# Kernel optimization log

Hardware: AMD Instinct MI355X
Metric: run time of the kernel (lower is better)

Reference implementation:

```python
import jax, jax.numpy as jnp
import numpy as np

N_NODES = 50000
N_EDGES = 800000
NUM_IN, NUM_OUT, NUM_HID, NUM_MSG = 1, 1, 30, 200


def _linear_params(key, fan_in, fan_out):
    k1, k2 = jax.random.split(key)
    s = 1.0 / np.sqrt(fan_in)
    W = jax.random.uniform(k1, (fan_in, fan_out), jnp.float32, -s, s)
    b = jax.random.uniform(k2, (fan_out,), jnp.float32, -s, s)
    return W, b


def _layer_params(key, c_in, c_out, c_msg):
    ks = jax.random.split(key, 4)
    W1, b1 = _linear_params(ks[0], c_in, c_out)          # lin_1
    Wm1, bm1 = _linear_params(ks[1], 2 * c_in + 2, c_msg)  # mlp[0]
    Wm2, bm2 = _linear_params(ks[2], c_msg, c_in)          # mlp[2]
    W2, b2 = _linear_params(ks[3], c_in, c_out)          # lin_2
    return W1, b1, Wm1, bm1, Wm2, bm2, W2, b2


def setup_inputs() -> dict:
    key = jax.random.key(0)
    ks = jax.random.split(key, 6)
    features = jax.random.normal(ks[0], (N_NODES, NUM_IN), jnp.float32)
    edges = jax.random.randint(ks[1], (2, N_EDGES), 0, N_NODES, jnp.int64)
    weights = jax.random.normal(ks[2], (N_EDGES, 2), jnp.float32)
    inp = {"features": features, "edges": edges, "weights": weights}
    names = ["W1", "b1", "Wm1", "bm1", "Wm2", "bm2", "W2", "b2"]
    for suf, kk, (ci, co) in zip(["d", "h", "o"], ks[3:6],
                                 [(NUM_IN, NUM_HID), (NUM_HID, NUM_HID), (NUM_HID, NUM_OUT)]):
        ps = _layer_params(kk, ci, co, NUM_MSG)
        for nm, p in zip(names, ps):
            inp[f"{nm}_{suf}"] = p
    return inp


def _mpd(x, src, dst, ea, W1, b1, Wm1, bm1, Wm2, bm2, W2, b2):
    # PyG default flow source_to_target: x_j = x[src], x_i = x[dst], aggregate to dst
    xi = x[dst]
    xj = x[src]
    tmp = jnp.concatenate([xi, xj, ea], axis=1)            # [E, 2*in+2]
    h = jax.nn.relu(tmp @ Wm1 + bm1)                       # [E, msg]
    m = h @ Wm2 + bm2                                      # [E, in]
    msg = (m * (xi - xj)) @ W2 + b2                        # [E, out]
    agg = jax.ops.segment_sum(msg, dst, num_segments=x.shape[0])
    return agg + x @ W1 + b1


def reference(features, edges, weights,
              W1_d, b1_d, Wm1_d, bm1_d, Wm2_d, bm2_d, W2_d, b2_d,
              W1_h, b1_h, Wm1_h, bm1_h, Wm2_h, bm2_h, W2_h, b2_h,
              W1_o, b1_o, Wm1_o, bm1_o, Wm2_o, bm2_o, W2_o, b2_o):
    src, dst = edges[0], edges[1]
    x = jax.nn.relu(_mpd(features, src, dst, weights,
                         W1_d, b1_d, Wm1_d, bm1_d, Wm2_d, bm2_d, W2_d, b2_d))
    for _ in range(3):
        x = jax.nn.relu(_mpd(x, src, dst, weights,
                             W1_h, b1_h, Wm1_h, bm1_h, Wm2_h, bm2_h, W2_h, b2_h))
    return _mpd(x, src, dst, weights,
                W1_o, b1_o, Wm1_o, bm1_o, Wm2_o, bm2_o, W2_o, b2_o)
```

## Files before the change

### kernel.cpp

```cpp
#include <hip/hip_runtime.h>

#define N_NODES 50000
#define N_EDGES 800000
#define C_MSG 200

typedef __bf16 bf16;
typedef __attribute__((ext_vector_type(8))) __bf16 bf16x8;
typedef __attribute__((ext_vector_type(4))) float f32x4;

static __device__ __forceinline__ unsigned int pk_bf16(float a, float b) {
    union { bf16 h[2]; unsigned int u; } cv;
    cv.h[0] = (bf16)a; cv.h[1] = (bf16)b;
    return cv.u;
}

static __device__ __forceinline__ f32x4 MF(bf16x8 a, bf16x8 b, f32x4 c) {
    return __builtin_amdgcn_mfma_f32_16x16x32_bf16(a, b, c, 0, 0, 0);
}

static __device__ void dev_pack_wm1(int tid, const float* W, const float* bm1,
                                    bf16* out) {
    int i = tid & 7, lane = (tid >> 3) & 63, rest = tid >> 9;
    int kt = rest % 2, t = rest / 2;
    int k = kt * 32 + ((lane >> 4) * 8) + i;
    int c = lane & 15;
    int n = (t < 12) ? ((t >> 1) * 32 + 2 * c + (t & 1)) : (192 + c);
    float v = 0.f;
    if (n < C_MSG) {
        if (k < 30)       v = W[k * C_MSG + n];
        else if (k == 30) v = bm1[n];
        else if (k >= 32) v = W[(k - 2) * C_MSG + n];
    }
    out[tid] = (bf16)v;
}

static __device__ void dev_pack_wm2(int tid, const float* W, const float* bm2,
                                    bf16* out) {
    int i = tid & 7, lane = (tid >> 3) & 63, rest = tid >> 9;
    int kt = rest % 7, nt = rest / 7;
    int k = kt * 32 + ((lane >> 4) * 8) + i;
    int n = 2 * (lane & 15) + nt;
    float v = 0.f;
    if (n < 30) {
        if (k < C_MSG)       v = W[k * 30 + n];
        else if (k == C_MSG) v = bm2[n];
    }
    out[tid] = (bf16)v;
}

static __device__ void dev_pack_w2h(int tid, const float* W, const float* b2,
                                    bf16* out) {
    int i = tid & 7, lane = (tid >> 3) & 63, nt = tid >> 9;
    int k = ((lane >> 4) * 8) + i;
    int n = 2 * (lane & 15) + nt;
    float v = 0.f;
    if (n < 30) {
        if (k < 30)       v = W[k * 30 + n];
        else if (k == 30) v = b2[n];
    }
    out[tid] = (bf16)v;
}

static __device__ void dev_pack_w2o(int tid, const float* W, const float* b2,
                                    bf16* out) {
    int i = tid & 7, lane = (tid >> 3) & 63;
    int k = ((lane >> 4) * 8) + i;
    int n = lane & 15;
    float v = 0.f;
    if (n == 0) {
        if (k < 30)       v = W[k];
        else if (k == 30) v = b2[0];
    }
    out[tid] = (bf16)v;
}

static __device__ void dev_pack_sel(int tid, bf16* out) {
    int i = tid & 7, lane = (tid >> 3) & 63, f = tid >> 9;
    int kt = f >> 1, nt = f & 1;
    int kloc = ((lane >> 4) * 8) + i;
    int n = 2 * (lane & 15) + nt;
    float v = (kloc == n && n < 30) ? ((kt & 1) ? -1.f : 1.f) : 0.f;
    out[tid] = (bf16)v;
}

__global__ __launch_bounds__(256) void setup_a(
    const int* __restrict__ dst, int* __restrict__ counts,
    const float* __restrict__ Wm1_h, const float* __restrict__ bm1_h,
    const float* __restrict__ Wm1_o, const float* __restrict__ bm1_o,
    const float* __restrict__ Wm2_h, const float* __restrict__ bm2_h,
    const float* __restrict__ Wm2_o, const float* __restrict__ bm2_o,
    const float* __restrict__ W2_h,  const float* __restrict__ b2_h,
    const float* __restrict__ W2_o,  const float* __restrict__ b2_o,
    const float* __restrict__ Wm1_d,
    bf16* __restrict__ Wm1B_h, bf16* __restrict__ Wm1B_o,
    bf16* __restrict__ Wm2B_h, bf16* __restrict__ Wm2B_o,
    bf16* __restrict__ W2B_h,  bf16* __restrict__ W2B_o,
    bf16* __restrict__ SelB,   float* __restrict__ Wm1T_d,
    const float* __restrict__ features, const float* __restrict__ W1_d,
    const float* __restrict__ b1_d, float* __restrict__ bufA) {
    int b = blockIdx.x, t = threadIdx.x;
    if (b < 3125) {
        int e = b * 256 + t;
        if (e < N_EDGES) atomicAdd(&counts[dst[e]], 1);
    } else if (b < 3311) {
        int pb = b - 3125;
        if (pb < 52)       dev_pack_wm1(pb * 256 + t, Wm1_h, bm1_h, Wm1B_h);
        else if (pb < 104) dev_pack_wm1((pb - 52) * 256 + t, Wm1_o, bm1_o, Wm1B_o);
        else if (pb < 132) dev_pack_wm2((pb - 104) * 256 + t, Wm2_h, bm2_h, Wm2B_h);
        else if (pb < 160) dev_pack_wm2((pb - 132) * 256 + t, Wm2_o, bm2_o, Wm2B_o);
        else if (pb < 164) dev_pack_w2h((pb - 160) * 256 + t, W2_h, b2_h, W2B_h);
        else if (pb < 166) dev_pack_w2o((pb - 164) * 256 + t, W2_o, b2_o, W2B_o);
        else if (pb < 182) dev_pack_sel((pb - 166) * 256 + t, SelB);
        else {
            int i = (pb - 182) * 256 + t;
            if (i < C_MSG * 4) Wm1T_d[i] = Wm1_d[(i & 3) * C_MSG + (i >> 2)];
        }
    } else {
        int n = (b - 3311) * 256 + t;
        if (n < N_NODES) {
            float xv = features[n];
            for (int o = 0; o < 30; ++o)
                bufA[n * 30 + o] = fmaf(xv, W1_d[o], b1_d[o]);
        }
    }
}

__global__ __launch_bounds__(256) void scan_kernel(const int* __restrict__ counts,
                                                   int* __restrict__ offsets,
                                                   int* __restrict__ cursor) {
    __shared__ int ws[4];
    const int b = blockIdx.x, t = threadIdx.x;
    const int lane = t & 63, wv = t >> 6;
    int acc = 0;
    for (int i = t; i < b * 256; i += 256) acc += counts[i];
#pragma unroll
    for (int d = 32; d > 0; d >>= 1) acc += __shfl_xor(acc, d);
    if (lane == 0) ws[wv] = acc;
    __syncthreads();
    int base = ws[0] + ws[1] + ws[2] + ws[3];
    __syncthreads();
    int i = b * 256 + t;
    int v = (i < N_NODES) ? counts[i] : 0;
    int inc = v;
#pragma unroll
    for (int d = 1; d < 64; d <<= 1) {
        int u = __shfl_up(inc, d);
        if (lane >= d) inc += u;
    }
    if (lane == 63) ws[wv] = inc;
    __syncthreads();
    int waveoff = 0;
    for (int k = 0; k < wv; ++k) waveoff += ws[k];
    int excl = base + waveoff + inc - v;
    if (i < N_NODES) { offsets[i] = excl; cursor[i] = excl; }
    if (i == N_NODES - 1) offsets[N_NODES] = excl + v;
}

__global__ __launch_bounds__(256) void scatter_kernel(
    const int* __restrict__ src, const int* __restrict__ dst,
    const float* __restrict__ ew, int* __restrict__ cursor,
    int4* __restrict__ edata, float2* __restrict__ ewp) {
    int e = blockIdx.x * 256 + threadIdx.x;
    if (e < N_EDGES) {
        int d = dst[e];
        float e0 = ew[2 * e], e1 = ew[2 * e + 1];
        int p = atomicAdd(&cursor[d], 1);
        edata[p] = make_int4(src[e], d, (int)pk_bf16(e0, e1), e);
        ewp[p] = make_float2(e0, e1);
    }
}

__global__ __launch_bounds__(256) void edge_d_kernel(
    const float* __restrict__ x, const int4* __restrict__ edata,
    const float2* __restrict__ ewp,
    const float* __restrict__ Wm1T, const float* __restrict__ bm1,
    const float* __restrict__ Wm2, const float* __restrict__ bm2,
    const float* __restrict__ W2, const float* __restrict__ b2, bf16* __restrict__ msg)
{
    int t = blockIdx.x * 256 + threadIdx.x;
    int4 ed = edata[t];
    float xi = x[ed.y], xj = x[ed.x];
    float2 e01 = ewp[t];
    float e0 = e01.x, e1 = e01.y;
    float m = bm2[0];
    for (int j = 0; j < C_MSG; ++j) {
        const float* __restrict__ wr = Wm1T + j * 4;
        float h = bm1[j];
        h = fmaf(xi, wr[0], h);
        h = fmaf(xj, wr[1], h);
        h = fmaf(e0, wr[2], h);
        h = fmaf(e1, wr[3], h);
        h = fmaxf(h, 0.f);
        m = fmaf(h, Wm2[j], m);
    }
    float md = m * (xi - xj);
    for (int o = 0; o < 15; ++o) {
        float f0 = fmaf(md, W2[2 * o], b2[2 * o]);
        float f1 = fmaf(md, W2[2 * o + 1], b2[2 * o + 1]);
        *(unsigned int*)(msg + (size_t)t * 32 + 2 * o) = pk_bf16(f0, f1);
    }
}


#define LOAD_FRAGS(P, ED) do {                                                \
    const bf16* rd_ = xc + (size_t)(ED).y * 64 + quad * 8;                    \
    const bf16* rs_ = xc + (size_t)(ED).x * 64 + quad * 8;                    \
    P##A0 = *(const bf16x8*)(rd_);                                            \
    P##a2 = *(const bf16x8*)(rd_ + 32);                                       \
    P##A1 = *(const bf16x8*)(rs_);                                            \
    P##a3 = *(const bf16x8*)(rs_ + 32);                                       \
} while (0)

#define COMPUTE_TILE(P, EDZ, EBASE) do {                                      \
    if (quad == 3) {                                                          \
        union { unsigned int u; bf16 b[2]; } cv_;                             \
        cv_.u = (unsigned int)(EDZ);                                          \
        P##A1[6] = cv_.b[0];                                                  \
        P##A1[7] = cv_.b[1];                                                  \
    }                                                                         \
               \
    f32x4 m0_ = {0.f,0.f,0.f,0.f}, m1_ = {0.f,0.f,0.f,0.f};                   \
    _Pragma("unroll")                                                         \
    for (int p_ = 0; p_ < 6; ++p_) {                                          \
        char* cb_ = (p_ & 1) ? cB : cA;                                       \
        const bf16* Wf_ = Wm1L + (4 * p_) * 512 + lane * 8;                   \
        bf16x8 be0_ = *(const bf16x8*)(Wf_);                                  \
        bf16x8 be1_ = *(const bf16x8*)(Wf_ + 512);                            \
        bf16x8 bo0_ = *(const bf16x8*)(Wf_ + 1024);                           \
        bf16x8 bo1_ = *(const bf16x8*)(Wf_ + 1536);                           \
        f32x4 ae_ = {0.f,0.f,0.f,0.f}, ao_ = {0.f,0.f,0.f,0.f};               \
        ae_ = MF(P##A0, be0_, ae_);                                           \
        ae_ = MF(P##A1, be1_, ae_);                                           \
        ao_ = MF(P##A0, bo0_, ao_);                                           \
        ao_ = MF(P##A1, bo1_, ao_);                                           \
        _Pragma("unroll")                                                     \
        for (int rg_ = 0; rg_ < 4; ++rg_) {                                   \
            int row_ = row0 + rg_, wb_ = 4 * col;                             \
            unsigned int u_ = pk_bf16(fmaxf(ae_[rg_],0.f), fmaxf(ao_[rg_],0.f)); \
            *(unsigned int*)(cb_ + row_ * 64 + ((wb_ & 48) ^ ((row_ & 3) << 4)) \
                             + (wb_ & 15)) = u_;                              \
        }                                                                     \
        bf16x8 a_ = *(const bf16x8*)(cb_ + col * 64 +                         \
                                     ((quad << 4) ^ ((col & 3) << 4)));       \
        m0_ = MF(a_, *(const bf16x8*)(Wm2L + p_ * 512 + lane * 8), m0_);      \
        m1_ = MF(a_, *(const bf16x8*)(Wm2L + (7 + p_) * 512 + lane * 8), m1_);\
    }                                                                         \
    {     \
        const bf16* Wf_ = Wm1L + 24 * 512 + lane * 8;                         \
        bf16x8 b0_ = *(const bf16x8*)(Wf_);                                   \
        bf16x8 b1_ = *(const bf16x8*)(Wf_ + 512);                             \
        f32x4 acc_ = {0.f,0.f,0.f,0.f};                                       \
        acc_ = MF(P##A0, b0_, acc_);                                          \
        acc_ = MF(P##A1, b1_, acc_);                                          \
        if (col < 8) {                                                        \
            _Pragma("unroll")                                                 \
            for (int rg_ = 0; rg_ < 4; ++rg_) {                               \
                int row_ = row0 + rg_;                                        \
                *(bf16*)(cP + row_ * 64 + ((row_ & 3) << 4) + 2 * col) =      \
                    (bf16)fmaxf(acc_[rg_], 0.f);                              \
            }                                                                 \
        }                                                                     \
        bf16x8 a_ = *(const bf16x8*)(cP + col * 64 +                          \
                                     ((quad << 4) ^ ((col & 3) << 4)));       \
        m0_ = MF(a_, *(const bf16x8*)(Wm2L + 6 * 512 + lane * 8), m0_);       \
        m1_ = MF(a_, *(const bf16x8*)(Wm2L + 13 * 512 + lane * 8), m1_);      \
    }                                                                         \
          \
    f32x4 dc0_ = {0.f,0.f,0.f,0.f}, dc1_ = {0.f,0.f,0.f,0.f};                 \
    dc0_ = MF(P##A0, *(const bf16x8*)(SelB + (size_t)0*512 + lane*8), dc0_);  \
    dc1_ = MF(P##A0, *(const bf16x8*)(SelB + (size_t)1*512 + lane*8), dc1_);  \
    dc0_ = MF(P##A1, *(const bf16x8*)(SelB + (size_t)2*512 + lane*8), dc0_);  \
    dc1_ = MF(P##A1, *(const bf16x8*)(SelB + (size_t)3*512 + lane*8), dc1_);  \
    dc0_ = MF(P##a2, *(const bf16x8*)(SelB + (size_t)4*512 + lane*8), dc0_);  \
    dc1_ = MF(P##a2, *(const bf16x8*)(SelB + (size_t)5*512 + lane*8), dc1_);  \
    dc0_ = MF(P##a3, *(const bf16x8*)(SelB + (size_t)6*512 + lane*8), dc0_);  \
    dc1_ = MF(P##a3, *(const bf16x8*)(SelB + (size_t)7*512 + lane*8), dc1_);  \
                                   \
    _Pragma("unroll")                                                         \
    for (int rg_ = 0; rg_ < 4; ++rg_) {                                       \
        int row_ = row0 + rg_, wb_ = 4 * col;                                 \
        unsigned int u_ = (col == 15) ? pk_bf16(1.f, 0.f)                     \
                        : pk_bf16(m0_[rg_]*dc0_[rg_], m1_[rg_]*dc1_[rg_]);    \
        *(unsigned int*)(cA + row_ * 64 + ((wb_ & 48) ^ ((row_ & 3) << 4))    \
                         + (wb_ & 15)) = u_;                                  \
    }                                                                         \
    bf16x8 am_ = *(const bf16x8*)(cA + col * 64 +                             \
                                  ((quad << 4) ^ ((col & 3) << 4)));          \
                                      \
    if (COUT == 30) {                                                         \
        f32x4 c0_ = {0.f,0.f,0.f,0.f}, c1_ = {0.f,0.f,0.f,0.f};               \
        c0_ = MF(am_, *(const bf16x8*)(W2B + lane*8), c0_);                   \
        c1_ = MF(am_, *(const bf16x8*)(W2B + 512 + lane*8), c1_);             \
        _Pragma("unroll")                                                     \
        for (int rg_ = 0; rg_ < 4; ++rg_)                                     \
            *(unsigned int*)(msg + (size_t)((EBASE) + row0 + rg_)*32 + 2*col) = \
                pk_bf16(c0_[rg_], c1_[rg_]);                                  \
    } else {                                                                  \
                  \
        f32x4 c0_ = {0.f,0.f,0.f,0.f};                                        \
        c0_ = MF(am_, *(const bf16x8*)(W2B + lane*8), c0_);                   \
        if (col == 0) {                                                       \
            union { bf16 h[4]; unsigned long long u; } pk4_;                  \
            _Pragma("unroll")                                                 \
            for (int rg_ = 0; rg_ < 4; ++rg_) pk4_.h[rg_] = (bf16)c0_[rg_];   \
            *(unsigned long long*)(msg + ((EBASE) + row0)) = pk4_.u;          \
        }                                                                     \
    }                                                                         \
} while (0)

template<int COUT>
__global__ __launch_bounds__(256, 3) void edge_mfma(
    const bf16* __restrict__ xc, const int4* __restrict__ edata,
    const bf16* __restrict__ Wm1B, const bf16* __restrict__ SelB,
    const bf16* __restrict__ Wm2B, const bf16* __restrict__ W2B,
    bf16* __restrict__ msg)
{
    __shared__ __align__(16) bf16 smem[26624];
    bf16* Wm1L = smem;
    bf16* Wm2L = smem + 13312;

    const int tid = threadIdx.x, w = tid >> 6, lane = tid & 63;
    const int col = lane & 15, quad = lane >> 4, row0 = quad * 4;
    const int myrow = w * 16;
    const int blk = blockIdx.x * 256;

    const int eoff = myrow + col;
    int4 ed0 = edata[blk + 0 * 64 + eoff];
    int4 ed1 = edata[blk + 1 * 64 + eoff];
    int4 ed2 = edata[blk + 2 * 64 + eoff];
    int4 ed3 = edata[blk + 3 * 64 + eoff];

#pragma unroll
    for (int i = 0; i < 10; ++i) {
        int idx = tid + i * 256;
        bf16x8 v = (idx < 1664) ? *((const bf16x8*)Wm1B + idx)
                                : *((const bf16x8*)Wm2B + (idx - 1664));
        *((bf16x8*)smem + idx) = v;
    }
    __syncthreads();

    char* cbase = (char*)(smem + 20480 + w * 1536);
    char* cA = cbase;
    char* cB = cbase + 1024;
    char* cP = cbase + 2048;

    if (lane < 48) {
        int r = lane / 3, s = 1 + (lane - r * 3);
        bf16x8 z = {};
        if (s == 1) z[0] = (bf16)1.f;
        *(bf16x8*)(cP + r * 64 + ((s << 4) ^ ((r & 3) << 4))) = z;
    }

    bf16x8 pA0, pA1, pa2, pa3, qA0, qA1, qa2, qa3;
    LOAD_FRAGS(p, ed0);
    LOAD_FRAGS(q, ed1);

    COMPUTE_TILE(p, ed0.z, blk + 0 * 64 + myrow);
    LOAD_FRAGS(p, ed2);
    COMPUTE_TILE(q, ed1.z, blk + 1 * 64 + myrow);
    LOAD_FRAGS(q, ed3);
    COMPUTE_TILE(p, ed2.z, blk + 2 * 64 + myrow);
    COMPUTE_TILE(q, ed3.z, blk + 3 * 64 + myrow);
}

template<int CNEXT>
__global__ __launch_bounds__(256) void agg_fused(
    const bf16* __restrict__ msg, const int* __restrict__ offsets,
    const float* __restrict__ bufc,
    const float* __restrict__ W1n, const float* __restrict__ b1n,
    float* __restrict__ bufn,
    bf16* __restrict__ xc) {
    int gh = (blockIdx.x * 256 + threadIdx.x) >> 4;
    int lane = threadIdx.x & 15;
    int s0 = offsets[gh], s1 = offsets[gh + 1];
    float r0 = 0.f, r1 = 0.f;
    if (lane < 15) {
        float v0 = 0.f, v1 = 0.f;
        const unsigned int* mp =
            (const unsigned int*)(msg + (size_t)s0 * 32 + lane * 2);
        int cnt = s1 - s0, j = 0;
        for (; j + 4 <= cnt; j += 4) {
            unsigned int u0 = mp[(size_t)(j + 0) * 16];
            unsigned int u1 = mp[(size_t)(j + 1) * 16];
            unsigned int u2 = mp[(size_t)(j + 2) * 16];
            unsigned int u3 = mp[(size_t)(j + 3) * 16];
            union { unsigned int u; bf16 b[2]; } c0, c1, c2, c3;
            c0.u = u0; c1.u = u1; c2.u = u2; c3.u = u3;
            v0 += (float)c0.b[0]; v1 += (float)c0.b[1];
            v0 += (float)c1.b[0]; v1 += (float)c1.b[1];
            v0 += (float)c2.b[0]; v1 += (float)c2.b[1];
            v0 += (float)c3.b[0]; v1 += (float)c3.b[1];
        }
        for (; j < cnt; ++j) {
            union { unsigned int u; bf16 b[2]; } cv;
            cv.u = mp[(size_t)j * 16];
            v0 += (float)cv.b[0]; v1 += (float)cv.b[1];
        }
        float f0 = bufc[(size_t)gh * 30 + 2 * lane] + v0;
        float f1 = bufc[(size_t)gh * 30 + 2 * lane + 1] + v1;
        r0 = fmaxf(f0, 0.f);
        r1 = fmaxf(f1, 0.f);
        bf16 h0 = (bf16)r0, h1 = (bf16)r1;
        union { bf16 h[2]; unsigned int u; } hi;
        hi.h[0] = h0; hi.h[1] = h1;
        *(unsigned int*)(xc + (size_t)gh * 64 + 2 * lane) = hi.u;
        *(unsigned int*)(xc + (size_t)gh * 64 + 32 + 2 * lane) =
            pk_bf16(r0 - (float)h0, r1 - (float)h1);
    } else {
        *(unsigned int*)(xc + (size_t)gh * 64 + 30) = pk_bf16(1.f, 0.f);
        *(unsigned int*)(xc + (size_t)gh * 64 + 62) = 0u;
    }
    if (CNEXT == 30) {
        float acc0 = 0.f, acc1 = 0.f;
        if (lane < 15) { acc0 = b1n[2 * lane]; acc1 = b1n[2 * lane + 1]; }
        for (int k2 = 0; k2 < 15; ++k2) {
            float rk0 = __shfl(r0, k2, 16);
            float rk1 = __shfl(r1, k2, 16);
            if (lane < 15) {
                const float* w0 = W1n + (2 * k2) * 30 + 2 * lane;
                const float* w1 = W1n + (2 * k2 + 1) * 30 + 2 * lane;
                acc0 = fmaf(rk0, w0[0], acc0);
                acc1 = fmaf(rk0, w0[1], acc1);
                acc0 = fmaf(rk1, w1[0], acc0);
                acc1 = fmaf(rk1, w1[1], acc1);
            }
        }
        if (lane < 15) {
            bufn[(size_t)gh * 30 + 2 * lane] = acc0;
            bufn[(size_t)gh * 30 + 2 * lane + 1] = acc1;
        }
    } else {
        float acc = b1n[0];
        for (int k2 = 0; k2 < 15; ++k2) {
            float rk0 = __shfl(r0, k2, 16);
            float rk1 = __shfl(r1, k2, 16);
            acc = fmaf(rk0, W1n[2 * k2], acc);
            acc = fmaf(rk1, W1n[2 * k2 + 1], acc);
        }
        if (lane == 0) bufn[gh] = acc;
    }
}

__global__ __launch_bounds__(256) void agg_last(const bf16* __restrict__ msg1,
                                                const int* __restrict__ offsets,
                                                float* __restrict__ out) {
    int gh = (blockIdx.x * 256 + threadIdx.x) >> 5;
    int lane = threadIdx.x & 31;
    int s0 = offsets[gh], s1 = offsets[gh + 1];
    float v = 0.f;
    for (int j = s0 + lane; j < s1; j += 32) v += (float)msg1[j];
#pragma unroll
    for (int o = 16; o > 0; o >>= 1) v += __shfl_xor(v, o);
    if (lane == 0) out[gh] += v;
}

extern "C" void kernel_launch(void* const* d_in, const int* in_sizes, int n_in,
                              void* d_out, int out_size, void* d_ws, size_t ws_size,
                              hipStream_t stream) {
    const float* features = (const float*)d_in[0];
    const int*   edges    = (const int*)d_in[1];
    const float* ew       = (const float*)d_in[2];

    const float* W1_d  = (const float*)d_in[3];
    const float* b1_d  = (const float*)d_in[4];
    const float* Wm1_d = (const float*)d_in[5];
    const float* bm1_d = (const float*)d_in[6];
    const float* Wm2_d = (const float*)d_in[7];
    const float* bm2_d = (const float*)d_in[8];
    const float* W2_d  = (const float*)d_in[9];
    const float* b2_d  = (const float*)d_in[10];

    const float* W1_h  = (const float*)d_in[11];
    const float* b1_h  = (const float*)d_in[12];
    const float* Wm1_h = (const float*)d_in[13];
    const float* bm1_h = (const float*)d_in[14];
    const float* Wm2_h = (const float*)d_in[15];
    const float* bm2_h = (const float*)d_in[16];
    const float* W2_h  = (const float*)d_in[17];
    const float* b2_h  = (const float*)d_in[18];

    const float* W1_o  = (const float*)d_in[19];
    const float* b1_o  = (const float*)d_in[20];
    const float* Wm1_o = (const float*)d_in[21];
    const float* bm1_o = (const float*)d_in[22];
    const float* Wm2_o = (const float*)d_in[23];
    const float* bm2_o = (const float*)d_in[24];
    const float* W2_o  = (const float*)d_in[25];
    const float* b2_o  = (const float*)d_in[26];

    const int* src = edges;
    const int* dst = edges + N_EDGES;
    float* out = (float*)d_out;

    char* p = (char*)d_ws;
    auto alloc = [&](size_t bytes) { char* r = p; p += (bytes + 63) & ~(size_t)63; return r; };
    float* bufA    = (float*)alloc((size_t)N_NODES * 30 * 4);
    float* bufB    = (float*)alloc((size_t)N_NODES * 30 * 4);
    bf16*  msg     = (bf16*) alloc((size_t)N_EDGES * 32 * 2);
    bf16*  xc      = (bf16*) alloc((size_t)N_NODES * 64 * 2);
    int*   counts  = (int*)  alloc((size_t)N_NODES * 4);
    int*   offsets = (int*)  alloc((size_t)(N_NODES + 1) * 4);
    int*   cursor  = (int*)  alloc((size_t)N_NODES * 4);
    int4*  edata   = (int4*) alloc((size_t)N_EDGES * 16);
    float2* ewp    = (float2*)alloc((size_t)N_EDGES * 8);
    float* Wm1T_d  = (float*)alloc((size_t)C_MSG * 4 * 4);
    bf16*  Wm1B_h  = (bf16*) alloc((size_t)26 * 512 * 2);
    bf16*  Wm1B_o  = (bf16*) alloc((size_t)26 * 512 * 2);
    bf16*  Wm2B_h  = (bf16*) alloc((size_t)14 * 512 * 2);
    bf16*  Wm2B_o  = (bf16*) alloc((size_t)14 * 512 * 2);
    bf16*  W2B_h   = (bf16*) alloc((size_t)2 * 512 * 2);
    bf16*  W2B_o   = (bf16*) alloc((size_t)1 * 512 * 2);
    bf16*  SelB    = (bf16*) alloc((size_t)8 * 512 * 2);

    hipMemsetAsync(counts, 0, (size_t)N_NODES * 4, stream);
    setup_a<<<3507, 256, 0, stream>>>(dst, counts,
        Wm1_h, bm1_h, Wm1_o, bm1_o, Wm2_h, bm2_h, Wm2_o, bm2_o,
        W2_h, b2_h, W2_o, b2_o, Wm1_d,
        Wm1B_h, Wm1B_o, Wm2B_h, Wm2B_o, W2B_h, W2B_o, SelB, Wm1T_d,
        features, W1_d, b1_d, bufA);
    scan_kernel<<<(N_NODES + 255) / 256, 256, 0, stream>>>(counts, offsets, cursor);
    scatter_kernel<<<N_EDGES / 256, 256, 0, stream>>>(src, dst, ew, cursor, edata, ewp);

    dim3 tb(256);
    dim3 eb_mfma(N_EDGES / 256);
    dim3 eb_valu(N_EDGES / 256);
    dim3 ab16(N_NODES * 16 / 256);
    dim3 ab32(N_NODES * 32 / 256);

    edge_d_kernel<<<eb_valu, tb, 0, stream>>>(features, edata, ewp,
        Wm1T_d, bm1_d, Wm2_d, bm2_d, W2_d, b2_d, msg);
    agg_fused<30><<<ab16, tb, 0, stream>>>(msg, offsets, bufA, W1_h, b1_h, bufB, xc);

    edge_mfma<30><<<eb_mfma, tb, 0, stream>>>(xc, edata,
        Wm1B_h, SelB, Wm2B_h, W2B_h, msg);
    agg_fused<30><<<ab16, tb, 0, stream>>>(msg, offsets, bufB, W1_h, b1_h, bufA, xc);

    edge_mfma<30><<<eb_mfma, tb, 0, stream>>>(xc, edata,
        Wm1B_h, SelB, Wm2B_h, W2B_h, msg);
    agg_fused<30><<<ab16, tb, 0, stream>>>(msg, offsets, bufA, W1_h, b1_h, bufB, xc);

    edge_mfma<30><<<eb_mfma, tb, 0, stream>>>(xc, edata,
        Wm1B_h, SelB, Wm2B_h, W2B_h, msg);
    agg_fused<1><<<ab16, tb, 0, stream>>>(msg, offsets, bufB, W1_o, b1_o, out, xc);

    edge_mfma<1><<<eb_mfma, tb, 0, stream>>>(xc, edata,
        Wm1B_o, SelB, Wm2B_o, W2B_o, msg);
    agg_last<<<ab32, tb, 0, stream>>>(msg, offsets, out);
}
```

Baseline: 581.6 us.

## Double edges per MFMA block, stage layer-d weights in LDS, unroll aggregation

The MFMA edge kernel now handles 512 edges per block instead of 256, so the LDS weight preload and setup are amortized over twice as many tiles. The edata and msg buffers are padded and zero-filled so the last block can safely read past the edge count. The first-layer VALU edge kernel stages its MLP weights in shared memory instead of reading them from global memory inside the loop. The aggregation loop gains an 8-way unrolled path for more loads in flight. In exchange, the MFMA grid halves, which lowers parallelism and extends each block's serial chain of tiles.

```diff
diff --git a/kernel.cpp b/kernel.cpp
--- a/kernel.cpp
+++ b/kernel.cpp
@@ -177,21 +177,33 @@
     const float* __restrict__ Wm2, const float* __restrict__ bm2,
     const float* __restrict__ W2, const float* __restrict__ b2, bf16* __restrict__ msg)
 {
+    __shared__ float sw[C_MSG * 6 + 1];
+    for (int i = threadIdx.x; i < C_MSG * 6 + 1; i += 256) {
+        float v;
+        if (i < C_MSG * 4)            v = Wm1T[i];
+        else if (i < C_MSG * 5)       v = bm1[i - C_MSG * 4];
+        else if (i < C_MSG * 6)       v = Wm2[i - C_MSG * 5];
+        else                          v = bm2[0];
+        sw[i] = v;
+    }
+    __syncthreads();
+
     int t = blockIdx.x * 256 + threadIdx.x;
     int4 ed = edata[t];
     float xi = x[ed.y], xj = x[ed.x];
     float2 e01 = ewp[t];
     float e0 = e01.x, e1 = e01.y;
-    float m = bm2[0];
+    float m = sw[C_MSG * 6];
+#pragma unroll 4
     for (int j = 0; j < C_MSG; ++j) {
-        const float* __restrict__ wr = Wm1T + j * 4;
-        float h = bm1[j];
+        const float* wr = sw + j * 4;
+        float h = sw[C_MSG * 4 + j];
         h = fmaf(xi, wr[0], h);
         h = fmaf(xj, wr[1], h);
         h = fmaf(e0, wr[2], h);
         h = fmaf(e1, wr[3], h);
         h = fmaxf(h, 0.f);
-        m = fmaf(h, Wm2[j], m);
+        m = fmaf(h, sw[C_MSG * 5 + j], m);
     }
     float md = m * (xi - xj);
     for (int o = 0; o < 15; ++o) {
@@ -322,13 +334,17 @@
     const int tid = threadIdx.x, w = tid >> 6, lane = tid & 63;
     const int col = lane & 15, quad = lane >> 4, row0 = quad * 4;
     const int myrow = w * 16;
-    const int blk = blockIdx.x * 256;
+    const int blk = blockIdx.x * 512;
 
     const int eoff = myrow + col;
     int4 ed0 = edata[blk + 0 * 64 + eoff];
     int4 ed1 = edata[blk + 1 * 64 + eoff];
     int4 ed2 = edata[blk + 2 * 64 + eoff];
     int4 ed3 = edata[blk + 3 * 64 + eoff];
+    int4 ed4 = edata[blk + 4 * 64 + eoff];
+    int4 ed5 = edata[blk + 5 * 64 + eoff];
+    int4 ed6 = edata[blk + 6 * 64 + eoff];
+    int4 ed7 = edata[blk + 7 * 64 + eoff];
 
 #pragma unroll
     for (int i = 0; i < 10; ++i) {
@@ -360,7 +376,15 @@
     COMPUTE_TILE(q, ed1.z, blk + 1 * 64 + myrow);
     LOAD_FRAGS(q, ed3);
     COMPUTE_TILE(p, ed2.z, blk + 2 * 64 + myrow);
+    LOAD_FRAGS(p, ed4);
     COMPUTE_TILE(q, ed3.z, blk + 3 * 64 + myrow);
+    LOAD_FRAGS(q, ed5);
+    COMPUTE_TILE(p, ed4.z, blk + 4 * 64 + myrow);
+    LOAD_FRAGS(p, ed6);
+    COMPUTE_TILE(q, ed5.z, blk + 5 * 64 + myrow);
+    LOAD_FRAGS(q, ed7);
+    COMPUTE_TILE(p, ed6.z, blk + 6 * 64 + myrow);
+    COMPUTE_TILE(q, ed7.z, blk + 7 * 64 + myrow);
 }
 
 template<int CNEXT>
@@ -379,6 +403,27 @@
         const unsigned int* mp =
             (const unsigned int*)(msg + (size_t)s0 * 32 + lane * 2);
         int cnt = s1 - s0, j = 0;
+        for (; j + 8 <= cnt; j += 8) {
+            unsigned int u0 = mp[(size_t)(j + 0) * 16];
+            unsigned int u1 = mp[(size_t)(j + 1) * 16];
+            unsigned int u2 = mp[(size_t)(j + 2) * 16];
+            unsigned int u3 = mp[(size_t)(j + 3) * 16];
+            unsigned int u4 = mp[(size_t)(j + 4) * 16];
+            unsigned int u5 = mp[(size_t)(j + 5) * 16];
+            unsigned int u6 = mp[(size_t)(j + 6) * 16];
+            unsigned int u7 = mp[(size_t)(j + 7) * 16];
+            union { unsigned int u; bf16 b[2]; } c0, c1, c2, c3, c4, c5, c6, c7;
+            c0.u = u0; c1.u = u1; c2.u = u2; c3.u = u3;
+            c4.u = u4; c5.u = u5; c6.u = u6; c7.u = u7;
+            v0 += (float)c0.b[0]; v1 += (float)c0.b[1];
+            v0 += (float)c1.b[0]; v1 += (float)c1.b[1];
+            v0 += (float)c2.b[0]; v1 += (float)c2.b[1];
+            v0 += (float)c3.b[0]; v1 += (float)c3.b[1];
+            v0 += (float)c4.b[0]; v1 += (float)c4.b[1];
+            v0 += (float)c5.b[0]; v1 += (float)c5.b[1];
+            v0 += (float)c6.b[0]; v1 += (float)c6.b[1];
+            v0 += (float)c7.b[0]; v1 += (float)c7.b[1];
+        }
         for (; j + 4 <= cnt; j += 4) {
             unsigned int u0 = mp[(size_t)(j + 0) * 16];
             unsigned int u1 = mp[(size_t)(j + 1) * 16];
@@ -496,12 +541,12 @@
     auto alloc = [&](size_t bytes) { char* r = p; p += (bytes + 63) & ~(size_t)63; return r; };
     float* bufA    = (float*)alloc((size_t)N_NODES * 30 * 4);
     float* bufB    = (float*)alloc((size_t)N_NODES * 30 * 4);
-    bf16*  msg     = (bf16*) alloc((size_t)N_EDGES * 32 * 2);
+    bf16*  msg     = (bf16*) alloc((size_t)(N_EDGES + 256) * 32 * 2);
     bf16*  xc      = (bf16*) alloc((size_t)N_NODES * 64 * 2);
     int*   counts  = (int*)  alloc((size_t)N_NODES * 4);
     int*   offsets = (int*)  alloc((size_t)(N_NODES + 1) * 4);
     int*   cursor  = (int*)  alloc((size_t)N_NODES * 4);
-    int4*  edata   = (int4*) alloc((size_t)N_EDGES * 16);
+    int4*  edata   = (int4*) alloc((size_t)(N_EDGES + 256) * 16);
     float2* ewp    = (float2*)alloc((size_t)N_EDGES * 8);
     float* Wm1T_d  = (float*)alloc((size_t)C_MSG * 4 * 4);
     bf16*  Wm1B_h  = (bf16*) alloc((size_t)26 * 512 * 2);
@@ -513,6 +558,7 @@
     bf16*  SelB    = (bf16*) alloc((size_t)8 * 512 * 2);
 
     hipMemsetAsync(counts, 0, (size_t)N_NODES * 4, stream);
+    hipMemsetAsync(edata + N_EDGES, 0, (size_t)256 * 16, stream);
     setup_a<<<3507, 256, 0, stream>>>(dst, counts,
         Wm1_h, bm1_h, Wm1_o, bm1_o, Wm2_h, bm2_h, Wm2_o, bm2_o,
         W2_h, b2_h, W2_o, b2_o, Wm1_d,
@@ -522,7 +568,7 @@
     scatter_kernel<<<N_EDGES / 256, 256, 0, stream>>>(src, dst, ew, cursor, edata, ewp);
 
     dim3 tb(256);
-    dim3 eb_mfma(N_EDGES / 256);
+    dim3 eb_mfma((N_EDGES + 511) / 512);
     dim3 eb_valu(N_EDGES / 256);
     dim3 ab16(N_NODES * 16 / 256);
     dim3 ab32(N_NODES * 32 / 256);
```

Result: no change. 582.8 us (+0.2%).
